# Optimization experiments

Hardware: AMD Instinct MI355X
Metric: run time of the kernel (lower is better)

## Reference

```python
import jax, jax.numpy as jnp
import numpy as np

NUM_CHANNELS = 64
NUM_FILTERS = 2
B, H, W = 4, 256, 256
K_SLOTS = NUM_FILTERS * 9 + 1  # 19 (9 taps per filter + skip slot)


def setup_inputs() -> dict:
    key = jax.random.key(0)
    k1, k2, k3 = jax.random.split(key, 3)
    k = jax.random.normal(k1, (B, K_SLOTS, H, W), dtype=jnp.float32)
    x = jax.random.normal(k2, (B, NUM_FILTERS * NUM_CHANNELS, H, W), dtype=jnp.float32)
    skip = jax.random.normal(k3, (B, NUM_CHANNELS, H, W), dtype=jnp.float32)
    return {"k": k, "x": x, "skip": skip}


def _patches3x3(x):
    # x: [B, C, H, W] -> [B, C, 9, H, W]; matches F.unfold(kernel=3, pad=1)
    # reshaped to (B, C, 9, H, W): tap order is row-major (ki, kj).
    Bx, Cx, Hx, Wx = x.shape
    xp = jnp.pad(x, ((0, 0), (0, 0), (1, 1), (1, 1)))
    taps = [xp[:, :, i:i + Hx, j:j + Wx] for i in range(3) for j in range(3)]
    return jnp.stack(taps, axis=2)


def reference(k, x, skip):
    # per-filter 3x3 patches, concatenated along the tap/slot axis
    plist = [_patches3x3(x[:, f * NUM_CHANNELS:(f + 1) * NUM_CHANNELS])
             for f in range(NUM_FILTERS)]
    plist.append(skip[:, :, None])                 # skip slot: [B, C, 1, H, W]
    patches = jnp.concatenate(plist, axis=2)       # [B, C, 19, H, W]
    # per-pixel predicted kernel broadcast over channels, reduce over slots
    return jnp.sum(patches * k[:, None], axis=2)   # [B, C, H, W]
```

## Files before the change

kernel.cpp:

```cpp
#include <hip/hip_runtime.h>


constexpr int Hh = 256;
constexpr int Ww = 256;
constexpr int HW = Hh * Ww;
constexpr int C  = 64;
constexpr int NF = 2;
constexpr int KS = 19;

__global__ __launch_bounds__(256) void filt_kernel(
    const float* __restrict__ kk,
    const float* __restrict__ x,
    const float* __restrict__ skip,
    float* __restrict__ out) {
  const int bh  = blockIdx.x;
  const int b   = bh >> 8;
  const int h   = bh & 255;
  const int tid = threadIdx.x;
  const int wg  = tid & 63;
  const int cq  = tid >> 6;
  const int w0  = wg << 2;

  const float* kbase = kk + (size_t)b * KS * HW + (size_t)h * Ww + w0;
  float kv[KS][4];
#pragma unroll
  for (int s = 0; s < KS; ++s) {
    float4 t = *(const float4*)(kbase + (size_t)s * HW);
    kv[s][0] = t.x; kv[s][1] = t.y; kv[s][2] = t.z; kv[s][3] = t.w;
  }

  const float* xb = x    + (size_t)b * NF * C * HW;
  const float* sb = skip + (size_t)b * C * HW + (size_t)h * Ww + w0;
  float*       ob = out  + (size_t)b * C * HW + (size_t)h * Ww + w0;

  const bool wlo = (w0 > 0);
  const bool whi = (w0 + 4 < Ww);

  for (int ci = 0; ci < 16; ++ci) {
    const int c = cq * 16 + ci;

    float4 sv = *(const float4*)(sb + (size_t)c * HW);
    float acc[4] = { kv[18][0] * sv.x, kv[18][1] * sv.y,
                     kv[18][2] * sv.z, kv[18][3] * sv.w };

#pragma unroll
    for (int f = 0; f < NF; ++f) {
      const float* xc = xb + (size_t)(f * C + c) * HW;
#pragma unroll
      for (int ki = 0; ki < 3; ++ki) {
        const int hh = h + ki - 1;
        if (hh >= 0 && hh < Hh) {
          const float* xr = xc + (size_t)hh * Ww;
          float v[6];
          v[0] = wlo ? xr[w0 - 1] : 0.0f;
          float4 xm = *(const float4*)(xr + w0);
          v[1] = xm.x; v[2] = xm.y; v[3] = xm.z; v[4] = xm.w;
          v[5] = whi ? xr[w0 + 4] : 0.0f;
#pragma unroll
          for (int kj = 0; kj < 3; ++kj) {
            const int s = f * 9 + ki * 3 + kj;
#pragma unroll
            for (int p = 0; p < 4; ++p)
              acc[p] = fmaf(kv[s][p], v[p + kj], acc[p]);
          }
        }
      }
    }

    float4 o;
    o.x = acc[0]; o.y = acc[1]; o.z = acc[2]; o.w = acc[3];
    *(float4*)(ob + (size_t)c * HW) = o;
  }
}

extern "C" void kernel_launch(void* const* d_in, const int* in_sizes, int n_in,
                              void* d_out, int out_size, void* d_ws, size_t ws_size,
                              hipStream_t stream) {
  const float* kk = (const float*)d_in[0];
  const float* x  = (const float*)d_in[1];
  const float* sk = (const float*)d_in[2];
  float* out = (float*)d_out;

  dim3 grid(4 * Hh);
  dim3 block(256);
  filt_kernel<<<grid, block, 0, stream>>>(kk, x, sk, out);
}
```

Measured before the change: 303.1 us.

## Split channels across 4x more blocks, stage k in LDS, shuffle halo values

The grid grows from one block per (batch,row) to four, each covering 16 channels, so each wave handles 4 channels and issues those loads with more memory-level parallelism per thread. The per-pixel kernel weights are staged once in LDS and read back per tap, which saves registers. The scalar halo loads are replaced with cross-lane shuffles. The costs are that the k row is loaded by four blocks instead of one and each block now pays a __syncthreads.

Result: faster. 278.9 us (-8.0%).

```diff
diff --git a/kernel.cpp b/kernel.cpp
--- a/kernel.cpp
+++ b/kernel.cpp
@@ -13,63 +13,77 @@
     const float* __restrict__ x,
     const float* __restrict__ skip,
     float* __restrict__ out) {
-  const int bh  = blockIdx.x;
-  const int b   = bh >> 8;
-  const int h   = bh & 255;
-  const int tid = threadIdx.x;
-  const int wg  = tid & 63;
-  const int cq  = tid >> 6;
-  const int w0  = wg << 2;
+  const int blk  = blockIdx.x;
+  const int cg   = blk & 3;
+  const int h    = (blk >> 2) & 255;
+  const int b    = blk >> 10;
+  const int tid  = threadIdx.x;
+  const int lane = tid & 63;
+  const int wv   = tid >> 6;
+  const int w0   = lane << 2;
 
-  const float* kbase = kk + (size_t)b * KS * HW + (size_t)h * Ww + w0;
-  float kv[KS][4];
+  __shared__ float lds_k[KS][Ww];
+
+  const float* kb = kk + (size_t)b * KS * HW + (size_t)h * Ww;
+  for (int s = wv; s < KS; s += 4)
+    *(float4*)&lds_k[s][w0] = *(const float4*)(kb + (size_t)s * HW + w0);
+  __syncthreads();
+
+  const int c0 = cg * 16 + wv * 4;
+  const float* xb = x    + (size_t)b * NF * C * HW;
+  const float* sb = skip + ((size_t)b * C + c0) * HW + (size_t)h * Ww + w0;
+  float*       ob = out  + ((size_t)b * C + c0) * HW + (size_t)h * Ww + w0;
+
+  float4 k18 = *(const float4*)&lds_k[18][w0];
+  float acc[4][4];
 #pragma unroll
-  for (int s = 0; s < KS; ++s) {
-    float4 t = *(const float4*)(kbase + (size_t)s * HW);
-    kv[s][0] = t.x; kv[s][1] = t.y; kv[s][2] = t.z; kv[s][3] = t.w;
+  for (int ch = 0; ch < 4; ++ch) {
+    float4 sv = *(const float4*)(sb + (size_t)ch * HW);
+    acc[ch][0] = k18.x * sv.x; acc[ch][1] = k18.y * sv.y;
+    acc[ch][2] = k18.z * sv.z; acc[ch][3] = k18.w * sv.w;
   }
 
-  const float* xb = x    + (size_t)b * NF * C * HW;
-  const float* sb = skip + (size_t)b * C * HW + (size_t)h * Ww + w0;
-  float*       ob = out  + (size_t)b * C * HW + (size_t)h * Ww + w0;
+#pragma unroll
+  for (int f = 0; f < NF; ++f) {
+    const float* xf = xb + (size_t)(f * C + c0) * HW;
+#pragma unroll
+    for (int ki = 0; ki < 3; ++ki) {
+      const int hh = h + ki - 1;
+      if (hh < 0 || hh >= Hh) continue;
+      const float* xr = xf + (size_t)hh * Ww + w0;
 
-  const bool wlo = (w0 > 0);
-  const bool whi = (w0 + 4 < Ww);
-
-  for (int ci = 0; ci < 16; ++ci) {
-    const int c = cq * 16 + ci;
-
-    float4 sv = *(const float4*)(sb + (size_t)c * HW);
-    float acc[4] = { kv[18][0] * sv.x, kv[18][1] * sv.y,
-                     kv[18][2] * sv.z, kv[18][3] * sv.w };
-
+      float v[4][6];
 #pragma unroll
-    for (int f = 0; f < NF; ++f) {
-      const float* xc = xb + (size_t)(f * C + c) * HW;
+      for (int ch = 0; ch < 4; ++ch) {
+        float4 xm = *(const float4*)(xr + (size_t)ch * HW);
+        v[ch][1] = xm.x; v[ch][2] = xm.y; v[ch][3] = xm.z; v[ch][4] = xm.w;
+      }
 #pragma unroll
-      for (int ki = 0; ki < 3; ++ki) {
-        const int hh = h + ki - 1;
-        if (hh >= 0 && hh < Hh) {
-          const float* xr = xc + (size_t)hh * Ww;
-          float v[6];
-          v[0] = wlo ? xr[w0 - 1] : 0.0f;
-          float4 xm = *(const float4*)(xr + w0);
-          v[1] = xm.x; v[2] = xm.y; v[3] = xm.z; v[4] = xm.w;
-          v[5] = whi ? xr[w0 + 4] : 0.0f;
+      for (int ch = 0; ch < 4; ++ch) {
+        float lf = __shfl_up(v[ch][4], 1);
+        float rg = __shfl_down(v[ch][1], 1);
+        v[ch][0] = (lane == 0)  ? 0.0f : lf;
+        v[ch][5] = (lane == 63) ? 0.0f : rg;
+      }
 #pragma unroll
-          for (int kj = 0; kj < 3; ++kj) {
-            const int s = f * 9 + ki * 3 + kj;
+      for (int kj = 0; kj < 3; ++kj) {
+        const int s = f * 9 + ki * 3 + kj;
+        float4 kw = *(const float4*)&lds_k[s][w0];
 #pragma unroll
-            for (int p = 0; p < 4; ++p)
-              acc[p] = fmaf(kv[s][p], v[p + kj], acc[p]);
-          }
+        for (int ch = 0; ch < 4; ++ch) {
+          acc[ch][0] = fmaf(kw.x, v[ch][0 + kj], acc[ch][0]);
+          acc[ch][1] = fmaf(kw.y, v[ch][1 + kj], acc[ch][1]);
+          acc[ch][2] = fmaf(kw.z, v[ch][2 + kj], acc[ch][2]);
+          acc[ch][3] = fmaf(kw.w, v[ch][3 + kj], acc[ch][3]);
         }
       }
     }
+  }
 
-    float4 o;
-    o.x = acc[0]; o.y = acc[1]; o.z = acc[2]; o.w = acc[3];
-    *(float4*)(ob + (size_t)c * HW) = o;
+#pragma unroll
+  for (int ch = 0; ch < 4; ++ch) {
+    float4 o = make_float4(acc[ch][0], acc[ch][1], acc[ch][2], acc[ch][3]);
+    *(float4*)(ob + (size_t)ch * HW) = o;
   }
 }
 
@@ -81,7 +95,7 @@
   const float* sk = (const float*)d_in[2];
   float* out = (float*)d_out;
 
-  dim3 grid(4 * Hh);
+  dim3 grid(4 * Hh * 4);
   dim3 block(256);
   filt_kernel<<<grid, block, 0, stream>>>(kk, x, sk, out);
 }
```
